# Kernel tuning notes

Measured on AMD Instinct MI355X. Metric: run time of the kernel, lower is better.

The kernel has to match this reference:

```python
import jax, jax.numpy as jnp
import numpy as np

L = 8192            # sequence length
V = 100000          # vocab size
E = 256             # embedding dim
H = 512             # lstm hidden dim (bidirectional total)
HD = H // 2         # per-direction hidden
TAGS = 32
T = TAGS + 2        # tagset + START/STOP
START = T - 2       # START_TAG = -2
STOP = T - 1        # STOP_TAG = -1
NEG = -10000.0


def setup_inputs() -> dict:
    key = jax.random.key(0)
    ks = jax.random.split(key, 11)
    s = 0.05
    return {
        "input_words": jax.random.randint(ks[0], (L,), 0, V),
        "embed": jax.random.normal(ks[1], (V, E), dtype=jnp.float32) * s,
        "Wih_f": jax.random.normal(ks[2], (4 * HD, E), dtype=jnp.float32) * s,
        "Whh_f": jax.random.normal(ks[3], (4 * HD, HD), dtype=jnp.float32) * s,
        "b_f": jax.random.normal(ks[4], (4 * HD,), dtype=jnp.float32) * s,
        "Wih_b": jax.random.normal(ks[5], (4 * HD, E), dtype=jnp.float32) * s,
        "Whh_b": jax.random.normal(ks[6], (4 * HD, HD), dtype=jnp.float32) * s,
        "b_b": jax.random.normal(ks[7], (4 * HD,), dtype=jnp.float32) * s,
        "W_out": jax.random.normal(ks[8], (T, H), dtype=jnp.float32) * s,
        "b_out": jax.random.normal(ks[9], (T,), dtype=jnp.float32) * s,
        "transitions": jax.random.normal(ks[10], (T, T), dtype=jnp.float32),
    }


def _lstm_dir(x, Wih, Whh, b, reverse):
    # single-layer LSTM, one direction; torch gate order i, f, g, o
    def step(carry, xt):
        h, c = carry
        g = xt @ Wih.T + h @ Whh.T + b
        i, f, gg, o = jnp.split(g, 4)
        i = jax.nn.sigmoid(i)
        f = jax.nn.sigmoid(f)
        gg = jnp.tanh(gg)
        o = jax.nn.sigmoid(o)
        c = f * c + i * gg
        h = o * jnp.tanh(c)
        return (h, c), h

    init = (jnp.zeros((HD,), x.dtype), jnp.zeros((HD,), x.dtype))
    _, hs = jax.lax.scan(step, init, x, reverse=reverse)
    return hs  # (L, HD)


def _crf_marginals(feats, transitions):
    lse = jax.nn.logsumexp
    # forward algorithm: alpha_t[j] = lse_i(alpha_{t-1}[i] + trans[j,i]) + feat_t[j]
    def fstep(alpha, feat):
        new = lse(alpha[None, :] + transitions, axis=1) + feat
        return new, new

    alpha0 = jnp.full((T,), NEG, feats.dtype).at[START].set(0.0)
    alphaL, log_alpha = jax.lax.scan(fstep, alpha0, feats)  # (L, T)

    # backward algorithm, replicating repo's init: beta_L[j] = lse_i(trans[i, j])
    beta_last = lse(transitions, axis=0)

    # beta_t[j] = lse_i(beta_{t+1}[i] + feat_{t+1}[i] + trans[i, j])
    def bstep(beta, feat_next):
        new = lse((beta + feat_next)[:, None] + transitions, axis=0)
        return new, new

    _, betas = jax.lax.scan(bstep, beta_last, feats[1:], reverse=True)
    log_beta = jnp.concatenate([betas, beta_last[None]], axis=0)  # (L, T)
    return log_alpha + log_beta


def reference(input_words, embed, Wih_f, Whh_f, b_f, Wih_b, Whh_b, b_b,
              W_out, b_out, transitions):
    x = embed[input_words]                           # (L, E)
    hf = _lstm_dir(x, Wih_f, Whh_f, b_f, reverse=False)
    hb = _lstm_dir(x, Wih_b, Whh_b, b_b, reverse=True)
    lstm_out = jnp.concatenate([hf, hb], axis=-1)    # (L, H)
    feats = lstm_out @ W_out.T + b_out               # (L, T)
    score = _crf_marginals(feats, transitions)       # (L, T)
    tags = jnp.argmax(score, axis=1)                 # (L,)
    return score, tags
```

## Files before the change

### kernel.cpp

```cpp
#include <hip/hip_runtime.h>
#include <cstdint>
#include <cstddef>

#define LSEQ 8192
#define NT   34
#define NP   36
#define SCH  64
#define CCH  128
#define F_L2E 1.4426950408889634f
#define F_LN2 0.6931471805599453f

typedef int v4i __attribute__((ext_vector_type(4)));

__device__ __forceinline__ float ex2(float x){ return exp2f(x); }
__device__ __forceinline__ float lg2(float x){ return __log2f(x); }

__device__ __forceinline__ float sigf(float x){
  return __fdividef(1.f, 1.f + ex2(-F_L2E * x));
}
__device__ __forceinline__ float tanhf_fast(float x){
  return 1.f - __fdividef(2.f, ex2(2.f * F_L2E * x) + 1.f);
}

__device__ __forceinline__ void barrier_lds(){
  asm volatile("s_waitcnt lgkmcnt(0)\n\ts_barrier" ::: "memory");
}

__global__ void k_quant(const float* __restrict__ Whh_f,
                        const float* __restrict__ Whh_b,
                        int* __restrict__ Wq, float* __restrict__ facP){
  int bid = blockIdx.x;
  int dir = bid >> 10;
  int r   = bid & 1023;
  int i   = threadIdx.x;
  const float* W = (dir ? Whh_b : Whh_f) + r * 256 + i * 4;
  float w0 = W[0], w1 = W[1], w2 = W[2], w3 = W[3];
  float m = fmaxf(fmaxf(fabsf(w0), fabsf(w1)), fmaxf(fabsf(w2), fabsf(w3)));
  for (int s = 32; s; s >>= 1) m = fmaxf(m, __shfl_xor(m, s));
  float scale = (m > 0.f) ? m / 127.f : 1.f;
  float inv = __fdividef(1.f, scale);
  int q0 = (int)rintf(w0 * inv), q1 = (int)rintf(w1 * inv);
  int q2 = (int)rintf(w2 * inv), q3 = (int)rintf(w3 * inv);
  q0 = max(-127, min(127, q0)); q1 = max(-127, min(127, q1));
  q2 = max(-127, min(127, q2)); q3 = max(-127, min(127, q3));
  int p = (q0 & 255) | ((q1 & 255) << 8) | ((q2 & 255) << 16) | ((q3 & 255) << 24);
  Wq[(dir << 16) + (r << 6) + i] = p;
  if (i == 0) {
    int g = r >> 8, u = r & 255;
    facP[(dir << 10) + u * 4 + g] = scale * (1.f / 127.f);
  }
}

__global__ void k_gproj(const int* __restrict__ words,
                        const float* __restrict__ embed,
                        const float* __restrict__ Wih_f, const float* __restrict__ b_f,
                        const float* __restrict__ Wih_b, const float* __restrict__ b_b,
                        float* __restrict__ G_f, float* __restrict__ G_b){
  int dir = blockIdx.y;
  const float* Wih = dir ? Wih_b : Wih_f;
  const float* bb  = dir ? b_b  : b_f;
  float* G = dir ? G_b : G_f;
  int t0 = blockIdx.x * 16;
  int uu = threadIdx.x;
  __shared__ __align__(16) float X[16 * 256];
  for (int idx = threadIdx.x; idx < 16 * 256; idx += 256) {
    int tt = idx >> 8, e = idx & 255;
    X[idx] = embed[(size_t)words[t0 + tt] * 256 + e];
  }
  __syncthreads();
  const float4* X4 = (const float4*)X;
  const float4* Wr0 = (const float4*)(Wih + (size_t)(uu)       * 256);
  const float4* Wr1 = (const float4*)(Wih + (size_t)(uu + 256) * 256);
  const float4* Wr2 = (const float4*)(Wih + (size_t)(uu + 512) * 256);
  const float4* Wr3 = (const float4*)(Wih + (size_t)(uu + 768) * 256);
  float b0 = bb[uu], b1 = bb[uu + 256], b2 = bb[uu + 512], b3 = bb[uu + 768];
  for (int pass = 0; pass < 2; pass++) {
    float4 acc[8];
#pragma unroll
    for (int tt = 0; tt < 8; tt++) acc[tt] = make_float4(b0, b1, b2, b3);
    for (int eb = 0; eb < 64; eb++) {
      float4 w0 = Wr0[eb], w1 = Wr1[eb], w2 = Wr2[eb], w3 = Wr3[eb];
#pragma unroll
      for (int tt = 0; tt < 8; tt++) {
        float4 x = X4[(pass * 8 + tt) * 64 + eb];
        acc[tt].x += w0.x * x.x + w0.y * x.y + w0.z * x.z + w0.w * x.w;
        acc[tt].y += w1.x * x.x + w1.y * x.y + w1.z * x.z + w1.w * x.w;
        acc[tt].z += w2.x * x.x + w2.y * x.y + w2.z * x.z + w2.w * x.w;
        acc[tt].w += w3.x * x.x + w3.y * x.y + w3.z * x.z + w3.w * x.w;
      }
    }
#pragma unroll
    for (int tt = 0; tt < 8; tt++)
      *(float4*)(G + (size_t)(t0 + pass * 8 + tt) * 1024 + uu * 4) = acc[tt];
  }
}

__global__ __launch_bounds__(512, 2) void k_lstm3(const int* __restrict__ Wq,
                                                  const float* __restrict__ facP,
                                                  const float* __restrict__ G_f,
                                                  const float* __restrict__ G_b,
                                                  float* __restrict__ hf,
                                                  float* __restrict__ hb){
  int dir = blockIdx.x;
  const int* Wqd = Wq + (dir << 16);
  const float* G = dir ? G_b : G_f;
  float* hout = dir ? hb : hf;
  int tid = threadIdx.x;
  int w = tid >> 6, L = tid & 63;
  int m = L & 15, q = L >> 4, T = L & 7, col = L & 15;
  int u = w * 32 + T * 4 + q;

  __shared__ int h8[2 * 64];

  v4i afr[8][4];
#pragma unroll
  for (int t8 = 0; t8 < 8; t8++) {
    int r_orig = (m & 3) * 256 + (w * 32 + t8 * 4 + (m >> 2));
    const int* base = Wqd + r_orig * 64;
#pragma unroll
    for (int kt = 0; kt < 4; kt++) {
      int4 tmp = *(const int4*)(base + kt * 16 + q * 4);
      afr[t8][kt] = (v4i){tmp.x, tmp.y, tmp.z, tmp.w};
    }
  }
  float4 fv = *(const float4*)(facP + (dir << 10) + u * 4);
  int time0 = dir ? 8191 : 0;
  float4 gcur = *(const float4*)(G + (size_t)time0 * 1024 + u * 4);

  if (tid < 128) h8[tid] = 0;
  float c = 0.f;
  __syncthreads();

  for (int t = 0; t < 8192; t++) {
    int tn = (t + 1 < 8192) ? t + 1 : 8191;
    int time_n = dir ? (8191 - tn) : tn;
    float4 gnext = *(const float4*)(G + (size_t)time_n * 1024 + u * 4);

    int p = t & 1;
    const char* rb = (const char*)h8 + p * 256;
    v4i bfr[4];
#pragma unroll
    for (int kt = 0; kt < 4; kt++) {
      int4 tmp = *(const int4*)(rb + kt * 64 + q * 16);
      bfr[kt] = (v4i){tmp.x, tmp.y, tmp.z, tmp.w};
    }
    v4i acc[8];
#pragma unroll
    for (int t8 = 0; t8 < 8; t8++) {
      v4i a = (v4i){0, 0, 0, 0};
#pragma unroll
      for (int kt = 0; kt < 4; kt++)
        a = __builtin_amdgcn_mfma_i32_16x16x64_i8(afr[t8][kt], bfr[kt], a, 0, 0, 0);
      acc[t8] = a;
    }
    v4i x0 = (T & 1) ? acc[1] : acc[0];
    v4i x1 = (T & 1) ? acc[3] : acc[2];
    v4i x2 = (T & 1) ? acc[5] : acc[4];
    v4i x3 = (T & 1) ? acc[7] : acc[6];
    v4i y0 = (T & 2) ? x1 : x0;
    v4i y1 = (T & 2) ? x3 : x2;
    v4i d  = (T & 4) ? y1 : y0;

    float ri = (float)d[0] * fv.x + gcur.x;
    float rf = (float)d[1] * fv.y + gcur.y;
    float rg = (float)d[2] * fv.z + gcur.z;
    float ro = (float)d[3] * fv.w + gcur.w;
    float is = sigf(ri), fs = sigf(rf);
    float gt = tanhf_fast(rg), os = sigf(ro);
    c = fs * c + is * gt;
    float h = os * tanhf_fast(c);

    int time = dir ? (8191 - t) : t;
    if (col < 8) {
      hout[(size_t)time * 256 + u] = h;
      ((signed char*)h8)[(p ^ 1) * 256 + u] = (signed char)(int)rintf(h * 127.f);
    }
    gcur = gnext;
    barrier_lds();
  }
}

__global__ void k_feats(const float* __restrict__ hf, const float* __restrict__ hb,
                        const float* __restrict__ W_out, const float* __restrict__ b_out,
                        float* __restrict__ feats){
  int t0 = blockIdx.x * 16;
  for (int oi = threadIdx.x; oi < 16 * NT; oi += 256) {
    int tt = oi / NT;
    int tag = oi - tt * NT;
    int t = t0 + tt;
    const float4* w4 = (const float4*)(W_out + (size_t)tag * 512);
    const float4* a4 = (const float4*)(hf + (size_t)t * 256);
    const float4* c4 = (const float4*)(hb + (size_t)t * 256);
    float acc = b_out[tag];
    for (int k = 0; k < 64; k++) {
      float4 w = w4[k]; float4 h = a4[k];
      acc += w.x * h.x + w.y * h.y + w.z * h.z + w.w * h.w;
    }
    for (int k = 0; k < 64; k++) {
      float4 w = w4[64 + k]; float4 h = c4[k];
      acc += w.x * h.x + w.y * h.y + w.z * h.z + w.w * h.w;
    }
    feats[(size_t)t * NT + tag] = acc;
  }
}

__global__ __launch_bounds__(320) void k_crf_p1(const float* __restrict__ feats,
                                                const float* __restrict__ trans,
                                                float* __restrict__ Pg,
                                                float* __restrict__ rmaxG){
  int dir = blockIdx.x >> 7;
  int c   = blockIdx.x & (CCH - 1);
  int tid = threadIdx.x;
  int t0  = c * SCH;

  __shared__ __align__(16) float TRM[NT * NP];
  __shared__ float Fe[(SCH + 1) * NT];
  __shared__ __align__(16) float Pbuf[2][NT * NP];
  __shared__ float CM[NP];
  __shared__ float RMs[NT];

  for (int idx = tid; idx < NT * NT; idx += 320) {
    int j = idx / NT, k = idx - j * NT;
    float v = (dir == 0) ? trans[j * NT + k] : trans[k * NT + j];
    TRM[j * NP + k] = v * F_L2E;
  }
  for (int idx = tid; idx < (SCH + 1) * NT; idx += 320) {
    int s = idx / NT, j = idx - s * NT;
    int t = t0 + s; if (t > LSEQ - 1) t = LSEQ - 1;
    Fe[idx] = feats[(size_t)t * NT + j] * F_L2E;
  }
  for (int idx = tid; idx < NT * NP; idx += 320) {
    int k = idx / NP, i = idx - k * NP;
    Pbuf[0][idx] = (i < NT && i == k) ? 0.f : -1e30f;
  }
  if (tid < NP) CM[tid] = (tid < NT) ? 0.f : -1e30f;
  __syncthreads();
  if (tid < NT) {
    float m = -3e38f;
    for (int k = 0; k < NT; k++) m = fmaxf(m, TRM[tid * NP + k]);
    RMs[tid] = m;
  }
  __syncthreads();
  for (int idx = tid; idx < NT * NT; idx += 320) {
    int j = idx / NT, k = idx - j * NT;
    TRM[j * NP + k] -= RMs[j];
  }
  __syncthreads();

  int cur = 0;
  int j = tid / 9, g = tid - (tid / 9) * 9;
  bool act = (tid < 306);
  int i0 = 4 * g;

  for (int s = 0; s < SCH; s++) {
    int t = (dir == 0) ? (t0 + s) : (t0 + SCH - 1 - s);
    if (dir == 1 && t == LSEQ - 1) continue;
    const float* Pc = Pbuf[cur];
    float* Pn = Pbuf[cur ^ 1];
    if (act) {
      float cm0 = CM[i0], cm1 = CM[i0 + 1], cm2 = CM[i0 + 2], cm3 = CM[i0 + 3];
      float s0 = 0, s1 = 0, s2 = 0, s3 = 0;
      const float* trp = TRM + j * NP;
      const float* fep = Fe + (t + 1 - t0) * NT;
#pragma unroll
      for (int k = 0; k < NT; k++) {
        float trv = trp[k];
        if (dir == 1) trv += fep[k];
        float4 p = *(const float4*)&Pc[k * NP + i0];
        s0 += ex2(trv + p.x - cm0);
        s1 += ex2(trv + p.y - cm1);
        s2 += ex2(trv + p.z - cm2);
        s3 += ex2(trv + p.w - cm3);
      }
      float base = RMs[j] + ((dir == 0) ? Fe[(t - t0) * NT + j] : 0.f);
      float4 o;
      o.x = base + cm0 + lg2(s0);
      o.y = base + cm1 + lg2(s1);
      o.z = (i0 + 2 < NT) ? (base + cm2 + lg2(s2)) : -1e30f;
      o.w = (i0 + 3 < NT) ? (base + cm3 + lg2(s3)) : -1e30f;
      *(float4*)&Pn[j * NP + i0] = o;
    }
    __syncthreads();
    if (tid < NP) {
      float m = -3e38f;
      const float* colp = Pn + tid;
      for (int k = 0; k < NT; k++) m = fmaxf(m, colp[k * NP]);
      CM[tid] = m;
    }
    cur ^= 1;
    __syncthreads();
  }

  const float* Pf = Pbuf[cur];
  size_t base = (size_t)((dir << 7) + c) * (NT * NP);
  for (int idx = tid; idx < NT * NP; idx += 320)
    Pg[base + idx] = Pf[idx];
  if (tid < NT) {
    float m = -3e38f;
    for (int i = 0; i < NT; i++) m = fmaxf(m, Pf[tid * NP + i]);
    rmaxG[((dir << 7) + c) * NT + tid] = m;
  }
}

__global__ void k_crf_p2(const float* __restrict__ trans,
                         const float* __restrict__ Pg,
                         const float* __restrict__ rmaxG,
                         float* __restrict__ vIn){
  int dir = blockIdx.x;
  int lane = threadIdx.x;
  bool a = (lane < NT);
  int j = a ? lane : 0;
  __shared__ float V[NP];

  float v;
  if (dir == 0) {
    v = (lane == 32) ? 0.f : -10000.f * F_L2E;
  } else {
    float m = -3e38f;
    for (int i = 0; i < NT; i++) m = fmaxf(m, trans[i * NT + j]);
    float s = 0.f;
    for (int i = 0; i < NT; i++) s += ex2((trans[i * NT + j] - m) * F_L2E);
    v = m * F_L2E + lg2(s);
  }
  if (lane < NP) V[lane] = -1e30f;
  barrier_lds();
  if (a) V[j] = v;
  barrier_lds();
  float vm = a ? v : -3e38f;
  for (int off = 32; off; off >>= 1) vm = fmaxf(vm, __shfl_xor(vm, off));

  if (a) {
    int c0 = (dir == 0) ? 0 : (CCH - 1);
    vIn[((size_t)(dir << 7) + c0) * NP + j] = v;
  }

  for (int it = 0; it < CCH - 1; it++) {
    int c = (dir == 0) ? it : (CCH - 1 - it);
    const float* row = Pg + ((size_t)(dir << 7) + c) * (NT * NP) + j * NP;
    float rm = rmaxG[((dir << 7) + c) * NT + j];
    float m = rm + vm;
    float s = 0.f;
#pragma unroll
    for (int k = 0; k < NP; k += 4) {
      float4 p = *(const float4*)&row[k];
      s += ex2(p.x + V[k]     - m);
      s += ex2(p.y + V[k + 1] - m);
      s += ex2(p.z + V[k + 2] - m);
      s += ex2(p.w + V[k + 3] - m);
    }
    float nv = m + lg2(s);
    if (a) V[j] = nv;
    barrier_lds();
    float x = a ? nv : -3e38f;
    for (int off = 32; off; off >>= 1) x = fmaxf(x, __shfl_xor(x, off));
    vm = x;
    int cn = (dir == 0) ? (c + 1) : (c - 1);
    if (a) vIn[((size_t)(dir << 7) + cn) * NP + j] = nv;
  }
}

__global__ void k_crf_p3(const float* __restrict__ feats,
                         const float* __restrict__ trans,
                         const float* __restrict__ vIn,
                         float* __restrict__ wsA,
                         float* __restrict__ wsB){
  int dir = blockIdx.x >> 7;
  int c   = blockIdx.x & (CCH - 1);
  int lane = threadIdx.x;
  int t0 = c * SCH;
  bool a = (lane < NT);
  int j = a ? lane : 0;
  __shared__ float A[NP];
  __shared__ float U[NP];

  float trr[NT];
  float rm = -3e38f;
#pragma unroll
  for (int k = 0; k < NT; k++) {
    float vv = (dir == 0) ? trans[j * NT + k] : trans[k * NT + j];
    trr[k] = vv * F_L2E;
    rm = fmaxf(rm, trr[k]);
  }
  if (lane < NP) { A[lane] = -1e30f; U[lane] = -1e30f; }
  float v0 = vIn[((size_t)(dir << 7) + c) * NP + j];
  barrier_lds();
  if (a) A[j] = v0;
  barrier_lds();
  float am = a ? v0 : -3e38f;
  for (int off = 32; off; off >>= 1) am = fmaxf(am, __shfl_xor(am, off));

  if (dir == 0) {
    float fe = feats[(size_t)t0 * NT + j] * F_L2E;
    for (int s = 0; s < SCH; s++) {
      int t = t0 + s;
      int tn = (t + 1 < LSEQ) ? t + 1 : LSEQ - 1;
      float fe_n = feats[(size_t)tn * NT + j] * F_L2E;
      float m = rm + am;
      float ss = 0.f;
#pragma unroll
      for (int k = 0; k < NT; k++) ss += ex2(trr[k] + A[k] - m);
      float out = m + lg2(ss) + fe;
      if (a) wsA[(size_t)t * NT + j] = out * F_LN2;
      if (a) A[j] = out;
      barrier_lds();
      float x = a ? out : -3e38f;
      for (int off = 32; off; off >>= 1) x = fmaxf(x, __shfl_xor(x, off));
      am = x;
      fe = fe_n;
    }
  } else {
    float b = v0;
    int tfirst = t0 + SCH; if (tfirst > LSEQ - 1) tfirst = LSEQ - 1;
    float fe = feats[(size_t)tfirst * NT + j] * F_L2E;
    for (int s = 0; s < SCH; s++) {
      int t = t0 + SCH - 1 - s;
      float fe_n = feats[(size_t)t * NT + j] * F_L2E;
      float out;
      if (t == LSEQ - 1) {
        out = b;
      } else {
        if (a) U[j] = b + fe;
        barrier_lds();
        float um = a ? U[j] : -3e38f;
        for (int off = 32; off; off >>= 1) um = fmaxf(um, __shfl_xor(um, off));
        float m = rm + um;
        float ss = 0.f;
#pragma unroll
        for (int k = 0; k < NT; k++) ss += ex2(trr[k] + U[k] - m);
        out = m + lg2(ss);
        barrier_lds();
      }
      if (a) wsB[(size_t)t * NT + j] = out * F_LN2;
      b = out;
      fe = fe_n;
    }
  }
}

__global__ void k_finish(const float* __restrict__ wsA, const float* __restrict__ wsB,
                         float* __restrict__ out){
  int t = blockIdx.x * 256 + threadIdx.x;
  float m = -3e38f; int bi = 0;
  for (int i = 0; i < NT; i++) {
    float sc = wsA[(size_t)t * NT + i] + wsB[(size_t)t * NT + i];
    out[(size_t)t * NT + i] = sc;
    if (sc > m) { m = sc; bi = i; }
  }
  out[(size_t)LSEQ * NT + t] = (float)bi;
}

extern "C" void kernel_launch(void* const* d_in, const int* in_sizes, int n_in,
                              void* d_out, int out_size, void* d_ws, size_t ws_size,
                              hipStream_t stream) {
  const int*   words  = (const int*)  d_in[0];
  const float* embed  = (const float*)d_in[1];
  const float* Wih_f  = (const float*)d_in[2];
  const float* Whh_f  = (const float*)d_in[3];
  const float* b_f    = (const float*)d_in[4];
  const float* Wih_b  = (const float*)d_in[5];
  const float* Whh_b  = (const float*)d_in[6];
  const float* b_b    = (const float*)d_in[7];
  const float* W_out  = (const float*)d_in[8];
  const float* b_out  = (const float*)d_in[9];
  const float* trans  = (const float*)d_in[10];
  float* out = (float*)d_out;

  float* wsf = (float*)d_ws;
  size_t off = 0;
  float* G_f   = wsf + off; off += (size_t)LSEQ * 1024;
  float* G_b   = wsf + off; off += (size_t)LSEQ * 1024;
  float* hf    = wsf + off; off += (size_t)LSEQ * 256;
  float* hb    = wsf + off; off += (size_t)LSEQ * 256;
  float* feats = wsf + off; off += (size_t)LSEQ * NT + 16;
  float* wsA   = wsf + off; off += (size_t)LSEQ * NT + 16;
  float* wsB   = wsf + off; off += (size_t)LSEQ * NT + 16;
  float* facP  = wsf + off; off += 2048;
  int*   Wq    = (int*)(wsf + off); off += 2 * 1024 * 64;
  float* Pg    = G_f;
  float* rmaxG = G_f + 256 * (NT * NP);
  float* vIn   = rmaxG + 256 * NT + 32;

  k_quant<<<2048, 64, 0, stream>>>(Whh_f, Whh_b, Wq, facP);
  k_gproj<<<dim3(512, 2), 256, 0, stream>>>(words, embed, Wih_f, b_f, Wih_b, b_b, G_f, G_b);
  k_lstm3<<<2, 512, 0, stream>>>(Wq, facP, G_f, G_b, hf, hb);
  k_feats<<<512, 256, 0, stream>>>(hf, hb, W_out, b_out, feats);
  k_crf_p1<<<256, 320, 0, stream>>>(feats, trans, Pg, rmaxG);
  k_crf_p2<<<2, 64, 0, stream>>>(trans, Pg, rmaxG, vIn);
  k_crf_p3<<<256, 64, 0, stream>>>(feats, trans, vIn, wsA, wsB);
  k_finish<<<32, 256, 0, stream>>>(wsA, wsB, out);
}
```

Before: 9.312 ms.

## Replace MFMA recurrent matvec with per-row sdot4 in a 1024-thread LSTM kernel

```diff
diff --git a/kernel.cpp b/kernel.cpp
--- a/kernel.cpp
+++ b/kernel.cpp
@@ -10,7 +10,18 @@
 #define F_L2E 1.4426950408889634f
 #define F_LN2 0.6931471805599453f
 
-typedef int v4i __attribute__((ext_vector_type(4)));
+#if __has_builtin(__builtin_amdgcn_sdot4)
+#define DOT4(a,b,c) __builtin_amdgcn_sdot4((a),(b),(c),false)
+#else
+__device__ __forceinline__ int dot4_fb(int a,int b,int c){
+  c += (int)(signed char)(a & 0xff)        * (int)(signed char)(b & 0xff);
+  c += (int)(signed char)((a>>8) & 0xff)   * (int)(signed char)((b>>8) & 0xff);
+  c += (int)(signed char)((a>>16) & 0xff)  * (int)(signed char)((b>>16) & 0xff);
+  c += (a>>24) * (b>>24);
+  return c;
+}
+#define DOT4(a,b,c) dot4_fb((a),(b),(c))
+#endif
 
 __device__ __forceinline__ float ex2(float x){ return exp2f(x); }
 __device__ __forceinline__ float lg2(float x){ return __log2f(x); }
@@ -95,87 +106,75 @@
   }
 }
 
-__global__ __launch_bounds__(512, 2) void k_lstm3(const int* __restrict__ Wq,
-                                                  const float* __restrict__ facP,
-                                                  const float* __restrict__ G_f,
-                                                  const float* __restrict__ G_b,
-                                                  float* __restrict__ hf,
-                                                  float* __restrict__ hb){
+__global__ __launch_bounds__(1024) void k_lstm4(const int* __restrict__ Wq,
+                                                const float* __restrict__ facP,
+                                                const float* __restrict__ G_f,
+                                                const float* __restrict__ G_b,
+                                                float* __restrict__ hf,
+                                                float* __restrict__ hb){
   int dir = blockIdx.x;
   const int* Wqd = Wq + (dir << 16);
   const float* G = dir ? G_b : G_f;
   float* hout = dir ? hb : hf;
   int tid = threadIdx.x;
-  int w = tid >> 6, L = tid & 63;
-  int m = L & 15, q = L >> 4, T = L & 7, col = L & 15;
-  int u = w * 32 + T * 4 + q;
-
-  __shared__ int h8[2 * 64];
-
-  v4i afr[8][4];
-#pragma unroll
-  for (int t8 = 0; t8 < 8; t8++) {
-    int r_orig = (m & 3) * 256 + (w * 32 + t8 * 4 + (m >> 2));
-    const int* base = Wqd + r_orig * 64;
-#pragma unroll
-    for (int kt = 0; kt < 4; kt++) {
-      int4 tmp = *(const int4*)(base + kt * 16 + q * 4);
-      afr[t8][kt] = (v4i){tmp.x, tmp.y, tmp.z, tmp.w};
-    }
-  }
-  float4 fv = *(const float4*)(facP + (dir << 10) + u * 4);
+  int l = tid & 63;
+  int g = l & 3;
+  int u = tid >> 2;
+  int qbase = l & ~3;
+
+  __shared__ __align__(16) int h8[2 * 64];
+
+  int r = g * 256 + u;
+  const int4* wp = (const int4*)(Wqd + r * 64);
+  int4 wreg[16];
+#pragma unroll
+  for (int kt = 0; kt < 16; kt++) wreg[kt] = wp[kt];
+
+  float facv = facP[(dir << 10) + tid];
   int time0 = dir ? 8191 : 0;
-  float4 gcur = *(const float4*)(G + (size_t)time0 * 1024 + u * 4);
+  int time1 = dir ? 8190 : 1;
+  float gcur = G[(size_t)time0 * 1024 + tid];
+  float gnxt = G[(size_t)time1 * 1024 + tid];
 
   if (tid < 128) h8[tid] = 0;
   float c = 0.f;
   __syncthreads();
 
   for (int t = 0; t < 8192; t++) {
-    int tn = (t + 1 < 8192) ? t + 1 : 8191;
-    int time_n = dir ? (8191 - tn) : tn;
-    float4 gnext = *(const float4*)(G + (size_t)time_n * 1024 + u * 4);
+    int tn2 = (t + 2 < 8192) ? t + 2 : 8191;
+    int time2 = dir ? (8191 - tn2) : tn2;
+    float gpre = G[(size_t)time2 * 1024 + tid];
 
     int p = t & 1;
-    const char* rb = (const char*)h8 + p * 256;
-    v4i bfr[4];
-#pragma unroll
-    for (int kt = 0; kt < 4; kt++) {
-      int4 tmp = *(const int4*)(rb + kt * 64 + q * 16);
-      bfr[kt] = (v4i){tmp.x, tmp.y, tmp.z, tmp.w};
-    }
-    v4i acc[8];
-#pragma unroll
-    for (int t8 = 0; t8 < 8; t8++) {
-      v4i a = (v4i){0, 0, 0, 0};
-#pragma unroll
-      for (int kt = 0; kt < 4; kt++)
-        a = __builtin_amdgcn_mfma_i32_16x16x64_i8(afr[t8][kt], bfr[kt], a, 0, 0, 0);
-      acc[t8] = a;
-    }
-    v4i x0 = (T & 1) ? acc[1] : acc[0];
-    v4i x1 = (T & 1) ? acc[3] : acc[2];
-    v4i x2 = (T & 1) ? acc[5] : acc[4];
-    v4i x3 = (T & 1) ? acc[7] : acc[6];
-    v4i y0 = (T & 2) ? x1 : x0;
-    v4i y1 = (T & 2) ? x3 : x2;
-    v4i d  = (T & 4) ? y1 : y0;
-
-    float ri = (float)d[0] * fv.x + gcur.x;
-    float rf = (float)d[1] * fv.y + gcur.y;
-    float rg = (float)d[2] * fv.z + gcur.z;
-    float ro = (float)d[3] * fv.w + gcur.w;
+    const int4* hb4 = (const int4*)(h8 + p * 64);
+    int a0 = 0, a1 = 0, a2 = 0, a3 = 0;
+#pragma unroll
+    for (int kt = 0; kt < 16; kt++) {
+      int4 hv = hb4[kt];
+      a0 = DOT4(wreg[kt].x, hv.x, a0);
+      a1 = DOT4(wreg[kt].y, hv.y, a1);
+      a2 = DOT4(wreg[kt].z, hv.z, a2);
+      a3 = DOT4(wreg[kt].w, hv.w, a3);
+    }
+    int acc = (a0 + a1) + (a2 + a3);
+    float a = (float)acc * facv + gcur;
+
+    float ri = __shfl(a, qbase + 0);
+    float rf = __shfl(a, qbase + 1);
+    float rg = __shfl(a, qbase + 2);
+    float ro = __shfl(a, qbase + 3);
+
     float is = sigf(ri), fs = sigf(rf);
     float gt = tanhf_fast(rg), os = sigf(ro);
     c = fs * c + is * gt;
     float h = os * tanhf_fast(c);
 
     int time = dir ? (8191 - t) : t;
-    if (col < 8) {
+    if (g == 0) {
       hout[(size_t)time * 256 + u] = h;
       ((signed char*)h8)[(p ^ 1) * 256 + u] = (signed char)(int)rintf(h * 127.f);
     }
-    gcur = gnext;
+    gcur = gnxt; gnxt = gpre;
     barrier_lds();
   }
 }
@@ -482,7 +481,7 @@
 
   k_quant<<<2048, 64, 0, stream>>>(Whh_f, Whh_b, Wq, facP);
   k_gproj<<<dim3(512, 2), 256, 0, stream>>>(words, embed, Wih_f, b_f, Wih_b, b_b, G_f, G_b);
-  k_lstm3<<<2, 512, 0, stream>>>(Wq, facP, G_f, G_b, hf, hb);
+  k_lstm4<<<2, 1024, 0, stream>>>(Wq, facP, G_f, G_b, hf, hb);
   k_feats<<<512, 256, 0, stream>>>(hf, hb, W_out, b_out, feats);
   k_crf_p1<<<256, 320, 0, stream>>>(feats, trans, Pg, rmaxG);
   k_crf_p2<<<2, 64, 0, stream>>>(trans, Pg, rmaxG, vIn);
```

Result: slower. 13.73 ms (+47.4%).
